# Kernel optimization log

Hardware: AMD Instinct MI355X
Metric: run time of the kernel (lower is better)

## Reference

```python
import jax, jax.numpy as jnp
import numpy as np

D_MODEL = 64
HIDDEN = 64
N_HEADS = 4
HEAD_DIM = HIDDEN // N_HEADS  # 16
MAX_LEN = 128
LN_EPS = 1e-5


def setup_inputs() -> dict:
    key = jax.random.key(0)
    ks = jax.random.split(key, 16)
    B, Lh, Lp = 4096, 128, 32
    s = 0.02
    return {
        "hla_out": jax.random.normal(ks[0], (B, Lh, D_MODEL), jnp.float32),
        "pep_out": jax.random.normal(ks[1], (B, Lp, D_MODEL), jnp.float32),
        "W_hla": jax.random.normal(ks[2], (D_MODEL, HIDDEN), jnp.float32) * s,
        "b_hla": jnp.zeros((HIDDEN,), jnp.float32),
        "W_pep": jax.random.normal(ks[3], (D_MODEL, HIDDEN), jnp.float32) * s,
        "b_pep": jnp.zeros((HIDDEN,), jnp.float32),
        "rel_bias": jax.random.normal(ks[4], (N_HEADS, MAX_LEN, MAX_LEN), jnp.float32) * s,
        "ln_g": jnp.ones((HIDDEN,), jnp.float32),
        "ln_b": jnp.zeros((HIDDEN,), jnp.float32),
        "W1": jax.random.normal(ks[5], (HIDDEN, 2 * HIDDEN), jnp.float32) * s,
        "b1": jnp.zeros((2 * HIDDEN,), jnp.float32),
        "W2": jax.random.normal(ks[6], (2 * HIDDEN, HIDDEN), jnp.float32) * s,
        "b2": jnp.zeros((HIDDEN,), jnp.float32),
        "W_out": jax.random.normal(ks[7], (HIDDEN, D_MODEL), jnp.float32) * s,
        "b_out": jnp.zeros((D_MODEL,), jnp.float32),
    }


def _layernorm(x, g, b):
    mu = jnp.mean(x, axis=-1, keepdims=True)
    var = jnp.mean(jnp.square(x - mu), axis=-1, keepdims=True)
    return (x - mu) * jax.lax.rsqrt(var + LN_EPS) * g + b


def reference(hla_out, pep_out, W_hla, b_hla, W_pep, b_pep, rel_bias,
              ln_g, ln_b, W1, b1, W2, b2, W_out, b_out):
    B, Lh, _ = hla_out.shape
    Lp = pep_out.shape[1]
    hla = hla_out @ W_hla + b_hla              # [B, Lh, HIDDEN]
    pep = pep_out @ W_pep + b_pep              # [B, Lp, HIDDEN]
    q = hla.reshape(B, Lh, N_HEADS, HEAD_DIM)
    kv = pep.reshape(B, Lp, N_HEADS, HEAD_DIM)  # k and v share projection
    scale = 1.0 / np.sqrt(HEAD_DIM).astype(np.float32)
    # [B, H, Lh, Lp]
    scores = jnp.einsum('bqhd,bkhd->bhqk', q, kv) * scale
    scores = scores + rel_bias[:, :Lh, :Lp]
    attn = jax.nn.softmax(scores, axis=-1)
    ctx = jnp.einsum('bhqk,bkhd->bqhd', attn, kv).reshape(B, Lh, HIDDEN)
    h = _layernorm(ctx, ln_g, ln_b)
    h = jax.nn.gelu(h @ W1 + b1, approximate=False) @ W2 + b2
    hla2pep = hla + h                          # residual onto projected hla
    return hla2pep @ W_out + b_out             # [B, Lh, D_MODEL]
```

## Files before the change

### kernel.cpp

```cpp
#include <hip/hip_runtime.h>

#define DEV static __device__ __forceinline__

using bf16x8 = __attribute__((ext_vector_type(8))) short;
using bf16x4 = __attribute__((ext_vector_type(4))) short;
using f32x4  = __attribute__((ext_vector_type(4))) float;
using f32x16 = __attribute__((ext_vector_type(16))) float;

DEV unsigned short f2bf(float f){
  unsigned u = __float_as_uint(f);
  return (unsigned short)((u + 0x7fffu + ((u >> 16) & 1u)) >> 16);
}
DEV float bf2f(unsigned short h){ return __uint_as_float(((unsigned)h) << 16); }

DEV float gelu_f(float x){
  float t  = 0.7978845608028654f * (x + 0.044715f * x * x * x);
  float e  = __expf(2.0f * t);
  float th = 1.0f - __fdividef(2.0f, e + 1.0f);
  return 0.5f * x * (1.0f + th);
}

__global__ void pack_weights(const float* __restrict__ Wh, const float* __restrict__ Wp,
                             const float* __restrict__ W1, const float* __restrict__ W2,
                             const float* __restrict__ Wo, const float* __restrict__ RB,
                             unsigned short* __restrict__ ws)
{
  const int gid = blockIdx.x * 256 + threadIdx.x;
  const float* W; unsigned short* o; int N, NB, idx;
  if      (gid < 4096)  { W = Wh; o = ws;         N = 64;  NB = 4; idx = gid;         }
  else if (gid < 8192)  { W = Wp; o = ws + 4096;  N = 64;  NB = 4; idx = gid - 4096;  }
  else if (gid < 16384) { W = W1; o = ws + 8192;  N = 128; NB = 8; idx = gid - 8192;  }
  else if (gid < 24576) { W = W2; o = ws + 16384; N = 64;  NB = 4; idx = gid - 16384; }
  else if (gid < 28672) { W = Wo; o = ws + 24576; N = 64;  NB = 4; idx = gid - 24576; }
  else {
    const int idx2 = gid - 28672;
    const int r = idx2 & 15, l = (idx2 >> 4) & 63, fid = idx2 >> 10;
    const int qt = fid & 3, h = fid >> 2;
    const int q  = qt * 32 + (l & 31);
    const int kp = (r & 3) + 8 * (r >> 2) + 4 * (l >> 5);
    ws[28672 + idx2] = f2bf(RB[((size_t)h * 128 + q) * 128 + kp]);
    return;
  }
  const int e = idx & 7, l = (idx >> 3) & 63, fid = idx >> 9;
  const int kb = fid / NB, nb = fid % NB;
  const int k  = kb * 32 + ((l >> 4) & 3) * 8 + e;
  const int n  = nb * 16 + (l & 15);
  o[idx] = f2bf(W[k * N + n]);
}

__global__ __launch_bounds__(256, 2)
void fused_kernel(const float* __restrict__ hla_in, const float* __restrict__ pep_in,
                  const float* __restrict__ bhla_p, const float* __restrict__ bpep_p,
                  const float* __restrict__ lng_p,  const float* __restrict__ lnb_p,
                  const float* __restrict__ b1_p,   const float* __restrict__ b2_p,
                  const float* __restrict__ bout_p,
                  const unsigned short* __restrict__ pk,
                  float* __restrict__ out)
{
  __shared__ __align__(16) unsigned char lds[56832];
  const int b   = blockIdx.x;
  const int tid = threadIdx.x;
  const int w   = tid >> 6;
  const int l   = tid & 63;
  const int li  = l & 15, l4 = l >> 4;
  const int lq  = l & 31, l5 = l >> 5;
  const int R0  = 32 * w;

  const unsigned short* pWh = pk;
  const unsigned short* pWp = pk + 4096;
  const unsigned short* pW1 = pk + 8192;
  const unsigned short* pW2 = pk + 16384;
  const unsigned short* pWo = pk + 24576;
  const unsigned short* pRB = pk + 28672;

  {
    const int mt = w & 1, np = w >> 1;
    bf16x8 aP[2];
#pragma unroll
    for (int kb = 0; kb < 2; ++kb){
      const float* s = pep_in + ((size_t)b * 32 + 16 * mt + li) * 64 + kb * 32 + l4 * 8;
      f32x4 u0 = *(const f32x4*)s;
      f32x4 u1 = *(const f32x4*)(s + 4);
      bf16x8 a;
      a[0] = (short)f2bf(u0[0]); a[1] = (short)f2bf(u0[1]);
      a[2] = (short)f2bf(u0[2]); a[3] = (short)f2bf(u0[3]);
      a[4] = (short)f2bf(u1[0]); a[5] = (short)f2bf(u1[1]);
      a[6] = (short)f2bf(u1[2]); a[7] = (short)f2bf(u1[3]);
      aP[kb] = a;
    }
#pragma unroll
    for (int t = 0; t < 2; ++t){
      const int nt = 2 * np + t;
      f32x4 acc = {0.f, 0.f, 0.f, 0.f};
#pragma unroll
      for (int kb = 0; kb < 2; ++kb){
        bf16x8 wf = *(const bf16x8*)(pWp + (size_t)((kb * 4 + nt) * 64 + l) * 8);
        acc = __builtin_amdgcn_mfma_f32_16x16x32_bf16(aP[kb], wf, acc, 0, 0, 0);
      }
      const float bp = bpep_p[nt * 16 + li];
#pragma unroll
      for (int r = 0; r < 4; ++r){
        const int row = 16 * mt + l4 * 4 + r;
        const int col = nt * 16 + li;
        const unsigned short v = f2bf(acc[r] + bp);
        *(unsigned short*)(lds + 36864 + row * 144 + col * 2) = v;
        *(unsigned short*)(lds + 41472 + col * 80 + row * 2) = v;
      }
    }
  }

  {
    bf16x8 aH[2][2];
#pragma unroll
    for (int ms = 0; ms < 2; ++ms)
#pragma unroll
    for (int kb = 0; kb < 2; ++kb){
      const float* s = hla_in + ((size_t)b * 128 + R0 + ms * 16 + li) * 64 + kb * 32 + l4 * 8;
      f32x4 u0 = *(const f32x4*)s;
      f32x4 u1 = *(const f32x4*)(s + 4);
      bf16x8 a;
      a[0] = (short)f2bf(u0[0]); a[1] = (short)f2bf(u0[1]);
      a[2] = (short)f2bf(u0[2]); a[3] = (short)f2bf(u0[3]);
      a[4] = (short)f2bf(u1[0]); a[5] = (short)f2bf(u1[1]);
      a[6] = (short)f2bf(u1[2]); a[7] = (short)f2bf(u1[3]);
      aH[ms][kb] = a;
    }
#pragma unroll
    for (int nt = 0; nt < 4; ++nt){
      f32x4 acc0 = {0.f, 0.f, 0.f, 0.f};
      f32x4 acc1 = {0.f, 0.f, 0.f, 0.f};
#pragma unroll
      for (int kb = 0; kb < 2; ++kb){
        bf16x8 wf = *(const bf16x8*)(pWh + (size_t)((kb * 4 + nt) * 64 + l) * 8);
        acc0 = __builtin_amdgcn_mfma_f32_16x16x32_bf16(aH[0][kb], wf, acc0, 0, 0, 0);
        acc1 = __builtin_amdgcn_mfma_f32_16x16x32_bf16(aH[1][kb], wf, acc1, 0, 0, 0);
      }
      const float bh = bhla_p[nt * 16 + li];
#pragma unroll
      for (int r = 0; r < 4; ++r){
        int row = R0 + l4 * 4 + r;
        *(unsigned short*)(lds + row * 144 + (nt * 16 + li) * 2) = f2bf(acc0[r] + bh);
        row += 16;
        *(unsigned short*)(lds + row * 144 + (nt * 16 + li) * 2) = f2bf(acc1[r] + bh);
      }
    }
  }

  __syncthreads();

  f32x4 ctxacc[2][4];
#pragma unroll
  for (int ms = 0; ms < 2; ++ms)
#pragma unroll
  for (int h = 0; h < 4; ++h){
    f32x4 z = {0.f, 0.f, 0.f, 0.f};
    ctxacc[ms][h] = z;
  }
  const unsigned lds_P = 46592 + (unsigned)w * 2560;

#pragma unroll
  for (int h = 0; h < 4; ++h){
    bf16x8 kvA = *(const bf16x8*)(lds + 36864 + lq * 144 + h * 32 + l5 * 16);
    bf16x8 qB  = *(const bf16x8*)(lds + (R0 + lq) * 144 + h * 32 + l5 * 16);
    f32x16 z16;
#pragma unroll
    for (int i = 0; i < 16; ++i) z16[i] = 0.f;
    f32x16 sc = __builtin_amdgcn_mfma_f32_32x32x16_bf16(kvA, qB, z16, 0, 0, 0);

    const unsigned short* rb = pRB + (size_t)((h * 4 + w) * 64 + l) * 16;
    bf16x8 r0 = *(const bf16x8*)rb;
    bf16x8 r1 = *(const bf16x8*)(rb + 8);
    float p[16];
#pragma unroll
    for (int i = 0; i < 8; ++i){
      p[i]     = sc[i]     * 0.25f + bf2f((unsigned short)r0[i]);
      p[i + 8] = sc[i + 8] * 0.25f + bf2f((unsigned short)r1[i]);
    }
    float mx = p[0];
#pragma unroll
    for (int i = 1; i < 16; ++i) mx = fmaxf(mx, p[i]);
    mx = fmaxf(mx, __shfl_xor(mx, 32));
    float sum = 0.f;
#pragma unroll
    for (int i = 0; i < 16; ++i){ p[i] = __expf(p[i] - mx); sum += p[i]; }
    sum += __shfl_xor(sum, 32);
    const float rs = __fdividef(1.0f, sum);

#pragma unroll
    for (int qd = 0; qd < 4; ++qd){
      bf16x4 v;
#pragma unroll
      for (int j = 0; j < 4; ++j) v[j] = (short)f2bf(p[qd * 4 + j] * rs);
      *(bf16x4*)(lds + lds_P + lq * 80 + (8 * qd + 4 * l5) * 2) = v;
    }
    asm volatile("" ::: "memory");

    bf16x8 bPV = *(const bf16x8*)(lds + 41472 + (h * 16 + li) * 80 + l4 * 16);
#pragma unroll
    for (int ms = 0; ms < 2; ++ms){
      bf16x8 aPV = *(const bf16x8*)(lds + lds_P + (ms * 16 + li) * 80 + l4 * 16);
      ctxacc[ms][h] = __builtin_amdgcn_mfma_f32_16x16x32_bf16(aPV, bPV, ctxacc[ms][h], 0, 0, 0);
    }
    asm volatile("" ::: "memory");
  }

  float gl[4], blv[4];
#pragma unroll
  for (int h = 0; h < 4; ++h){ gl[h] = lng_p[h * 16 + li]; blv[h] = lnb_p[h * 16 + li]; }
#pragma unroll
  for (int ms = 0; ms < 2; ++ms)
#pragma unroll
  for (int r = 0; r < 4; ++r){
    float x0 = ctxacc[ms][0][r], x1 = ctxacc[ms][1][r];
    float x2 = ctxacc[ms][2][r], x3 = ctxacc[ms][3][r];
    float t = x0 + x1 + x2 + x3;
    t += __shfl_xor(t, 1); t += __shfl_xor(t, 2);
    t += __shfl_xor(t, 4); t += __shfl_xor(t, 8);
    const float mean = t * 0.015625f;
    x0 -= mean; x1 -= mean; x2 -= mean; x3 -= mean;
    float v = x0 * x0 + x1 * x1 + x2 * x2 + x3 * x3;
    v += __shfl_xor(v, 1); v += __shfl_xor(v, 2);
    v += __shfl_xor(v, 4); v += __shfl_xor(v, 8);
    const float rstd = rsqrtf(v * 0.015625f + 1e-5f);
    const int row = R0 + ms * 16 + l4 * 4 + r;
    *(unsigned short*)(lds + 18432 + row * 144 + (li) * 2)      = f2bf(x0 * rstd * gl[0] + blv[0]);
    *(unsigned short*)(lds + 18432 + row * 144 + (16 + li) * 2) = f2bf(x1 * rstd * gl[1] + blv[1]);
    *(unsigned short*)(lds + 18432 + row * 144 + (32 + li) * 2) = f2bf(x2 * rstd * gl[2] + blv[2]);
    *(unsigned short*)(lds + 18432 + row * 144 + (48 + li) * 2) = f2bf(x3 * rstd * gl[3] + blv[3]);
  }

  __syncthreads();

  bf16x8 aX[2][2];
#pragma unroll
  for (int ms = 0; ms < 2; ++ms)
#pragma unroll
  for (int kb = 0; kb < 2; ++kb)
    aX[ms][kb] = *(const bf16x8*)(lds + 18432 + (R0 + ms * 16 + li) * 144 + kb * 64 + l4 * 16);

  f32x4 acc4[2][4];
#pragma unroll
  for (int ms = 0; ms < 2; ++ms)
#pragma unroll
  for (int nt = 0; nt < 4; ++nt){
    f32x4 z = {0.f, 0.f, 0.f, 0.f};
    acc4[ms][nt] = z;
  }

#pragma unroll
  for (int half = 0; half < 2; ++half){
#pragma unroll
    for (int nt = 0; nt < 4; ++nt){
      f32x4 a30 = {0.f, 0.f, 0.f, 0.f};
      f32x4 a31 = {0.f, 0.f, 0.f, 0.f};
#pragma unroll
      for (int kb = 0; kb < 2; ++kb){
        bf16x8 wf = *(const bf16x8*)(pW1 + (size_t)((kb * 8 + half * 4 + nt) * 64 + l) * 8);
        a30 = __builtin_amdgcn_mfma_f32_16x16x32_bf16(aX[0][kb], wf, a30, 0, 0, 0);
        a31 = __builtin_amdgcn_mfma_f32_16x16x32_bf16(aX[1][kb], wf, a31, 0, 0, 0);
      }
      const float bb = b1_p[half * 64 + nt * 16 + li];
#pragma unroll
      for (int r = 0; r < 4; ++r){
        int row = R0 + l4 * 4 + r;
        *(unsigned short*)(lds + 36864 + row * 144 + (nt * 16 + li) * 2) = f2bf(gelu_f(a30[r] + bb));
        row += 16;
        *(unsigned short*)(lds + 36864 + row * 144 + (nt * 16 + li) * 2) = f2bf(gelu_f(a31[r] + bb));
      }
    }
    asm volatile("" ::: "memory");
    bf16x8 aT[2][2];
#pragma unroll
    for (int ms = 0; ms < 2; ++ms)
#pragma unroll
    for (int kb = 0; kb < 2; ++kb)
      aT[ms][kb] = *(const bf16x8*)(lds + 36864 + (R0 + ms * 16 + li) * 144 + kb * 64 + l4 * 16);
#pragma unroll
    for (int nt = 0; nt < 4; ++nt){
#pragma unroll
      for (int kb = 0; kb < 2; ++kb){
        bf16x8 wf = *(const bf16x8*)(pW2 + (size_t)(((half * 2 + kb) * 4 + nt) * 64 + l) * 8);
        acc4[0][nt] = __builtin_amdgcn_mfma_f32_16x16x32_bf16(aT[0][kb], wf, acc4[0][nt], 0, 0, 0);
        acc4[1][nt] = __builtin_amdgcn_mfma_f32_16x16x32_bf16(aT[1][kb], wf, acc4[1][nt], 0, 0, 0);
      }
    }
    asm volatile("" ::: "memory");
  }

#pragma unroll
  for (int nt = 0; nt < 4; ++nt){
    const float bb2 = b2_p[nt * 16 + li];
#pragma unroll
    for (int ms = 0; ms < 2; ++ms)
#pragma unroll
    for (int r = 0; r < 4; ++r){
      const int row = R0 + ms * 16 + l4 * 4 + r;
      const float hl = bf2f(*(const unsigned short*)(lds + row * 144 + (nt * 16 + li) * 2));
      *(unsigned short*)(lds + 18432 + row * 144 + (nt * 16 + li) * 2) =
          f2bf(acc4[ms][nt][r] + bb2 + hl);
    }
  }
  asm volatile("" ::: "memory");

  bf16x8 aO[2][2];
#pragma unroll
  for (int ms = 0; ms < 2; ++ms)
#pragma unroll
  for (int kb = 0; kb < 2; ++kb)
    aO[ms][kb] = *(const bf16x8*)(lds + 18432 + (R0 + ms * 16 + li) * 144 + kb * 64 + l4 * 16);

#pragma unroll
  for (int nt = 0; nt < 4; ++nt){
    f32x4 a50 = {0.f, 0.f, 0.f, 0.f};
    f32x4 a51 = {0.f, 0.f, 0.f, 0.f};
#pragma unroll
    for (int kb = 0; kb < 2; ++kb){
      bf16x8 wf = *(const bf16x8*)(pWo + (size_t)((kb * 4 + nt) * 64 + l) * 8);
      a50 = __builtin_amdgcn_mfma_f32_16x16x32_bf16(aO[0][kb], wf, a50, 0, 0, 0);
      a51 = __builtin_amdgcn_mfma_f32_16x16x32_bf16(aO[1][kb], wf, a51, 0, 0, 0);
    }
    const float bo = bout_p[nt * 16 + li];
#pragma unroll
    for (int r = 0; r < 4; ++r){
      int row = R0 + l4 * 4 + r;
      out[((size_t)b * 128 + row) * 64 + nt * 16 + li] = a50[r] + bo;
      row += 16;
      out[((size_t)b * 128 + row) * 64 + nt * 16 + li] = a51[r] + bo;
    }
  }
}

extern "C" void kernel_launch(void* const* d_in, const int* in_sizes, int n_in,
                              void* d_out, int out_size, void* d_ws, size_t ws_size,
                              hipStream_t stream)
{
  const float* hla  = (const float*)d_in[0];
  const float* pep  = (const float*)d_in[1];
  const float* Wh   = (const float*)d_in[2];
  const float* bhla = (const float*)d_in[3];
  const float* Wp   = (const float*)d_in[4];
  const float* bpep = (const float*)d_in[5];
  const float* RB   = (const float*)d_in[6];
  const float* lng  = (const float*)d_in[7];
  const float* lnb  = (const float*)d_in[8];
  const float* W1   = (const float*)d_in[9];
  const float* b1   = (const float*)d_in[10];
  const float* W2   = (const float*)d_in[11];
  const float* b2   = (const float*)d_in[12];
  const float* Wo   = (const float*)d_in[13];
  const float* bo   = (const float*)d_in[14];
  unsigned short* ws = (unsigned short*)d_ws;
  float* outp = (float*)d_out;

  hipLaunchKernelGGL(pack_weights, dim3(176), dim3(256), 0, stream,
                     Wh, Wp, W1, W2, Wo, RB, ws);
  hipLaunchKernelGGL(fused_kernel, dim3(4096), dim3(256), 0, stream,
                     hla, pep, bhla, bpep, lng, lnb, b1, b2, bo, ws, outp);
}
```

Baseline: 356.5 us.

## Shrink LDS to per-wave regions, raise occupancy, use exp2 softmax and residual-in-registers

Reorganizes shared memory into a small shared KV region plus per-wave private scratch (Q/X/P), cutting LDS from about 56.8KB to 38.4KB and raising launch bounds to 4 blocks per CU. The second block-wide barrier is removed because each wave now reuses only its own region. The hla projection is kept in fp32 accumulators and used as the initial value of the FFN output accumulator, so the residual no longer needs an LDS read. Softmax switches to exp2 with log2e folded into the scale and the packed rel_bias, GELU is rewritten in a cheaper sigmoid form, and float-to-bf16 uses the native conversion. Higher occupancy may force register spills under the tighter launch bound.

```diff
diff --git a/kernel.cpp b/kernel.cpp
--- a/kernel.cpp
+++ b/kernel.cpp
@@ -8,16 +8,16 @@
 using f32x16 = __attribute__((ext_vector_type(16))) float;
 
 DEV unsigned short f2bf(float f){
-  unsigned u = __float_as_uint(f);
-  return (unsigned short)((u + 0x7fffu + ((u >> 16) & 1u)) >> 16);
+  return __builtin_bit_cast(unsigned short, (__bf16)f);
 }
 DEV float bf2f(unsigned short h){ return __uint_as_float(((unsigned)h) << 16); }
 
 DEV float gelu_f(float x){
-  float t  = 0.7978845608028654f * (x + 0.044715f * x * x * x);
-  float e  = __expf(2.0f * t);
-  float th = 1.0f - __fdividef(2.0f, e + 1.0f);
-  return 0.5f * x * (1.0f + th);
+  float x2  = x * x;
+  float q   = __builtin_fmaf(0.044715f, x2, 1.0f);
+  float arg = 2.302208225f * (x * q);
+  float e   = __builtin_amdgcn_exp2f(arg);
+  return __fdividef(x * e, e + 1.0f);
 }
 
 __global__ void pack_weights(const float* __restrict__ Wh, const float* __restrict__ Wp,
@@ -38,7 +38,7 @@
     const int qt = fid & 3, h = fid >> 2;
     const int q  = qt * 32 + (l & 31);
     const int kp = (r & 3) + 8 * (r >> 2) + 4 * (l >> 5);
-    ws[28672 + idx2] = f2bf(RB[((size_t)h * 128 + q) * 128 + kp]);
+    ws[28672 + idx2] = f2bf(1.44269504f * RB[((size_t)h * 128 + q) * 128 + kp]);
     return;
   }
   const int e = idx & 7, l = (idx >> 3) & 63, fid = idx >> 9;
@@ -48,7 +48,10 @@
   o[idx] = f2bf(W[k * N + n]);
 }
 
-__global__ __launch_bounds__(256, 2)
+#define KV_OFF  0
+#define KVT_OFF 4608
+
+__global__ __launch_bounds__(256, 4)
 void fused_kernel(const float* __restrict__ hla_in, const float* __restrict__ pep_in,
                   const float* __restrict__ bhla_p, const float* __restrict__ bpep_p,
                   const float* __restrict__ lng_p,  const float* __restrict__ lnb_p,
@@ -57,7 +60,7 @@
                   const unsigned short* __restrict__ pk,
                   float* __restrict__ out)
 {
-  __shared__ __align__(16) unsigned char lds[56832];
+  __shared__ __align__(16) unsigned char lds[38400];
   const int b   = blockIdx.x;
   const int tid = threadIdx.x;
   const int w   = tid >> 6;
@@ -65,6 +68,8 @@
   const int li  = l & 15, l4 = l >> 4;
   const int lq  = l & 31, l5 = l >> 5;
   const int R0  = 32 * w;
+  const unsigned QX = 9728u + (unsigned)w * 7168u;
+  const unsigned PW = QX + 4608u;
 
   const unsigned short* pWh = pk;
   const unsigned short* pWp = pk + 4096;
@@ -103,12 +108,13 @@
         const int row = 16 * mt + l4 * 4 + r;
         const int col = nt * 16 + li;
         const unsigned short v = f2bf(acc[r] + bp);
-        *(unsigned short*)(lds + 36864 + row * 144 + col * 2) = v;
-        *(unsigned short*)(lds + 41472 + col * 80 + row * 2) = v;
-      }
-    }
-  }
-
+        *(unsigned short*)(lds + KV_OFF  + row * 144 + col * 2) = v;
+        *(unsigned short*)(lds + KVT_OFF + col * 80  + row * 2) = v;
+      }
+    }
+  }
+
+  f32x4 acc4[2][4];
   {
     bf16x8 aH[2][2];
 #pragma unroll
@@ -137,11 +143,15 @@
       }
       const float bh = bhla_p[nt * 16 + li];
 #pragma unroll
+      for (int r = 0; r < 4; ++r){ acc0[r] += bh; acc1[r] += bh; }
+      acc4[0][nt] = acc0;
+      acc4[1][nt] = acc1;
+#pragma unroll
       for (int r = 0; r < 4; ++r){
-        int row = R0 + l4 * 4 + r;
-        *(unsigned short*)(lds + row * 144 + (nt * 16 + li) * 2) = f2bf(acc0[r] + bh);
+        int row = l4 * 4 + r;
+        *(unsigned short*)(lds + QX + row * 144 + (nt * 16 + li) * 2) = f2bf(acc0[r]);
         row += 16;
-        *(unsigned short*)(lds + row * 144 + (nt * 16 + li) * 2) = f2bf(acc1[r] + bh);
+        *(unsigned short*)(lds + QX + row * 144 + (nt * 16 + li) * 2) = f2bf(acc1[r]);
       }
     }
   }
@@ -156,12 +166,11 @@
     f32x4 z = {0.f, 0.f, 0.f, 0.f};
     ctxacc[ms][h] = z;
   }
-  const unsigned lds_P = 46592 + (unsigned)w * 2560;
 
 #pragma unroll
   for (int h = 0; h < 4; ++h){
-    bf16x8 kvA = *(const bf16x8*)(lds + 36864 + lq * 144 + h * 32 + l5 * 16);
-    bf16x8 qB  = *(const bf16x8*)(lds + (R0 + lq) * 144 + h * 32 + l5 * 16);
+    bf16x8 kvA = *(const bf16x8*)(lds + KV_OFF + lq * 144 + h * 32 + l5 * 16);
+    bf16x8 qB  = *(const bf16x8*)(lds + QX     + lq * 144 + h * 32 + l5 * 16);
     f32x16 z16;
 #pragma unroll
     for (int i = 0; i < 16; ++i) z16[i] = 0.f;
@@ -173,8 +182,8 @@
     float p[16];
 #pragma unroll
     for (int i = 0; i < 8; ++i){
-      p[i]     = sc[i]     * 0.25f + bf2f((unsigned short)r0[i]);
-      p[i + 8] = sc[i + 8] * 0.25f + bf2f((unsigned short)r1[i]);
+      p[i]     = __builtin_fmaf(sc[i],     0.36067376f, bf2f((unsigned short)r0[i]));
+      p[i + 8] = __builtin_fmaf(sc[i + 8], 0.36067376f, bf2f((unsigned short)r1[i]));
     }
     float mx = p[0];
 #pragma unroll
@@ -182,7 +191,7 @@
     mx = fmaxf(mx, __shfl_xor(mx, 32));
     float sum = 0.f;
 #pragma unroll
-    for (int i = 0; i < 16; ++i){ p[i] = __expf(p[i] - mx); sum += p[i]; }
+    for (int i = 0; i < 16; ++i){ p[i] = __builtin_amdgcn_exp2f(p[i] - mx); sum += p[i]; }
     sum += __shfl_xor(sum, 32);
     const float rs = __fdividef(1.0f, sum);
 
@@ -191,14 +200,14 @@
       bf16x4 v;
 #pragma unroll
       for (int j = 0; j < 4; ++j) v[j] = (short)f2bf(p[qd * 4 + j] * rs);
-      *(bf16x4*)(lds + lds_P + lq * 80 + (8 * qd + 4 * l5) * 2) = v;
+      *(bf16x4*)(lds + PW + lq * 80 + (8 * qd + 4 * l5) * 2) = v;
     }
     asm volatile("" ::: "memory");
 
-    bf16x8 bPV = *(const bf16x8*)(lds + 41472 + (h * 16 + li) * 80 + l4 * 16);
+    bf16x8 bPV = *(const bf16x8*)(lds + KVT_OFF + (h * 16 + li) * 80 + l4 * 16);
 #pragma unroll
     for (int ms = 0; ms < 2; ++ms){
-      bf16x8 aPV = *(const bf16x8*)(lds + lds_P + (ms * 16 + li) * 80 + l4 * 16);
+      bf16x8 aPV = *(const bf16x8*)(lds + PW + (ms * 16 + li) * 80 + l4 * 16);
       ctxacc[ms][h] = __builtin_amdgcn_mfma_f32_16x16x32_bf16(aPV, bPV, ctxacc[ms][h], 0, 0, 0);
     }
     asm volatile("" ::: "memory");
@@ -222,30 +231,21 @@
     v += __shfl_xor(v, 1); v += __shfl_xor(v, 2);
     v += __shfl_xor(v, 4); v += __shfl_xor(v, 8);
     const float rstd = rsqrtf(v * 0.015625f + 1e-5f);
-    const int row = R0 + ms * 16 + l4 * 4 + r;
-    *(unsigned short*)(lds + 18432 + row * 144 + (li) * 2)      = f2bf(x0 * rstd * gl[0] + blv[0]);
-    *(unsigned short*)(lds + 18432 + row * 144 + (16 + li) * 2) = f2bf(x1 * rstd * gl[1] + blv[1]);
-    *(unsigned short*)(lds + 18432 + row * 144 + (32 + li) * 2) = f2bf(x2 * rstd * gl[2] + blv[2]);
-    *(unsigned short*)(lds + 18432 + row * 144 + (48 + li) * 2) = f2bf(x3 * rstd * gl[3] + blv[3]);
-  }
-
-  __syncthreads();
+    const int row = ms * 16 + l4 * 4 + r;
+    *(unsigned short*)(lds + QX + row * 144 + (li) * 2)      = f2bf(x0 * rstd * gl[0] + blv[0]);
+    *(unsigned short*)(lds + QX + row * 144 + (16 + li) * 2) = f2bf(x1 * rstd * gl[1] + blv[1]);
+    *(unsigned short*)(lds + QX + row * 144 + (32 + li) * 2) = f2bf(x2 * rstd * gl[2] + blv[2]);
+    *(unsigned short*)(lds + QX + row * 144 + (48 + li) * 2) = f2bf(x3 * rstd * gl[3] + blv[3]);
+  }
+  asm volatile("" ::: "memory");
 
   bf16x8 aX[2][2];
 #pragma unroll
   for (int ms = 0; ms < 2; ++ms)
 #pragma unroll
   for (int kb = 0; kb < 2; ++kb)
-    aX[ms][kb] = *(const bf16x8*)(lds + 18432 + (R0 + ms * 16 + li) * 144 + kb * 64 + l4 * 16);
-
-  f32x4 acc4[2][4];
-#pragma unroll
-  for (int ms = 0; ms < 2; ++ms)
-#pragma unroll
-  for (int nt = 0; nt < 4; ++nt){
-    f32x4 z = {0.f, 0.f, 0.f, 0.f};
-    acc4[ms][nt] = z;
-  }
+    aX[ms][kb] = *(const bf16x8*)(lds + QX + (ms * 16 + li) * 144 + kb * 64 + l4 * 16);
+  asm volatile("" ::: "memory");
 
 #pragma unroll
   for (int half = 0; half < 2; ++half){
@@ -262,10 +262,10 @@
       const float bb = b1_p[half * 64 + nt * 16 + li];
 #pragma unroll
       for (int r = 0; r < 4; ++r){
-        int row = R0 + l4 * 4 + r;
-        *(unsigned short*)(lds + 36864 + row * 144 + (nt * 16 + li) * 2) = f2bf(gelu_f(a30[r] + bb));
+        int row = l4 * 4 + r;
+        *(unsigned short*)(lds + QX + row * 144 + (nt * 16 + li) * 2) = f2bf(gelu_f(a30[r] + bb));
         row += 16;
-        *(unsigned short*)(lds + 36864 + row * 144 + (nt * 16 + li) * 2) = f2bf(gelu_f(a31[r] + bb));
+        *(unsigned short*)(lds + QX + row * 144 + (nt * 16 + li) * 2) = f2bf(gelu_f(a31[r] + bb));
       }
     }
     asm volatile("" ::: "memory");
@@ -274,7 +274,7 @@
     for (int ms = 0; ms < 2; ++ms)
 #pragma unroll
     for (int kb = 0; kb < 2; ++kb)
-      aT[ms][kb] = *(const bf16x8*)(lds + 36864 + (R0 + ms * 16 + li) * 144 + kb * 64 + l4 * 16);
+      aT[ms][kb] = *(const bf16x8*)(lds + QX + (ms * 16 + li) * 144 + kb * 64 + l4 * 16);
 #pragma unroll
     for (int nt = 0; nt < 4; ++nt){
 #pragma unroll
@@ -294,10 +294,9 @@
     for (int ms = 0; ms < 2; ++ms)
 #pragma unroll
     for (int r = 0; r < 4; ++r){
-      const int row = R0 + ms * 16 + l4 * 4 + r;
-      const float hl = bf2f(*(const unsigned short*)(lds + row * 144 + (nt * 16 + li) * 2));
-      *(unsigned short*)(lds + 18432 + row * 144 + (nt * 16 + li) * 2) =
-          f2bf(acc4[ms][nt][r] + bb2 + hl);
+      const int row = ms * 16 + l4 * 4 + r;
+      *(unsigned short*)(lds + QX + row * 144 + (nt * 16 + li) * 2) =
+          f2bf(acc4[ms][nt][r] + bb2);
     }
   }
   asm volatile("" ::: "memory");
@@ -307,8 +306,9 @@
   for (int ms = 0; ms < 2; ++ms)
 #pragma unroll
   for (int kb = 0; kb < 2; ++kb)
-    aO[ms][kb] = *(const bf16x8*)(lds + 18432 + (R0 + ms * 16 + li) * 144 + kb * 64 + l4 * 16);
-
+    aO[ms][kb] = *(const bf16x8*)(lds + QX + (ms * 16 + li) * 144 + kb * 64 + l4 * 16);
+
+  float* outb = out + (size_t)b * 8192 + (R0 + l4 * 4) * 64 + li;
 #pragma unroll
   for (int nt = 0; nt < 4; ++nt){
     f32x4 a50 = {0.f, 0.f, 0.f, 0.f};
@@ -322,10 +322,8 @@
     const float bo = bout_p[nt * 16 + li];
 #pragma unroll
     for (int r = 0; r < 4; ++r){
-      int row = R0 + l4 * 4 + r;
-      out[((size_t)b * 128 + row) * 64 + nt * 16 + li] = a50[r] + bo;
-      row += 16;
-      out[((size_t)b * 128 + row) * 64 + nt * 16 + li] = a51[r] + bo;
+      outb[r * 64 + nt * 16]        = a50[r] + bo;
+      outb[1024 + r * 64 + nt * 16] = a51[r] + bo;
     }
   }
 }
```

New measurement: 348.0 us. 1.02x faster.
